# Kernel optimization log

Hardware: AMD Instinct MI355X
Metric: run time of the kernel (lower is better)

The kernel has to match this reference:

```python
import jax, jax.numpy as jnp
import numpy as np

L, D, H, HK, DH, F, V, T, B = 8, 1024, 16, 4, 64, 2816, 32000, 1024, 2
G = H // HK
THETA = 10000.0
EPS = 1e-6
SCALE = DH ** -0.5


def _rope_tables(t, dh, theta):
    inv = 1.0 / theta ** (jnp.arange(0, dh, 2, dtype=jnp.float32) / dh)  # [dh/2]
    ang = jnp.arange(t, dtype=jnp.float32)[:, None] * inv[None, :]       # [T, dh/2]
    return jnp.cos(ang), jnp.sin(ang)


def _apply_rope(x, cos, sin):
    # x: [B, T, h, DH] -> rotate pairs (even, odd)
    xr = x.reshape(*x.shape[:-1], DH // 2, 2)
    x0, x1 = xr[..., 0], xr[..., 1]
    c = cos[None, :, None, :]
    s = sin[None, :, None, :]
    out = jnp.stack([x0 * c - x1 * s, x0 * s + x1 * c], axis=-1)
    return out.reshape(*x.shape)


def _rmsnorm(x, w):
    var = jnp.mean(x * x, axis=-1, keepdims=True)
    return x * jax.lax.rsqrt(var + EPS) * w


def setup_inputs() -> dict:
    key = jax.random.key(0)
    ks = jax.random.split(key, 10)
    s = 0.02
    return {
        "ids": jax.random.randint(ks[0], (B, T), 0, V),
        "emb": jax.random.normal(ks[1], (V, D), jnp.float32) * s,
        "qw": jax.random.normal(ks[2], (L, H * DH, D), jnp.float32) * s,
        "kw": jax.random.normal(ks[3], (L, HK * DH, D), jnp.float32) * s,
        "vw": jax.random.normal(ks[4], (L, HK * DH, D), jnp.float32) * s,
        "ow": jax.random.normal(ks[5], (L, D, D), jnp.float32) * s,
        "w1": jax.random.normal(ks[6], (L, F, D), jnp.float32) * s,
        "w2": jax.random.normal(ks[7], (L, D, F), jnp.float32) * s,
        "w3": jax.random.normal(ks[8], (L, F, D), jnp.float32) * s,
        "n1": jnp.ones((L, D), jnp.float32),
        "n2": jnp.ones((L, D), jnp.float32),
        "nf": jnp.ones((D,), jnp.float32),
    }


def _forward(ids, emb, qw, kw, vw, ow, w1, w2, w3, n1, n2, nf):
    cos, sin = _rope_tables(T, DH, THETA)
    causal = jnp.tril(jnp.ones((T, T), dtype=bool))  # [T, T]
    x = emb[ids]  # [B, T, D]
    for l in range(L):
        xn = _rmsnorm(x, n1[l])
        q = jnp.einsum("btd,ed->bte", xn, qw[l]).reshape(B, T, H, DH)
        k = jnp.einsum("btd,ed->bte", xn, kw[l]).reshape(B, T, HK, DH)
        v = jnp.einsum("btd,ed->bte", xn, vw[l]).reshape(B, T, HK, DH)
        q = _apply_rope(q, cos, sin)
        k = _apply_rope(k, cos, sin)
        # GQA: group query heads over shared kv heads
        qg = q.transpose(0, 2, 1, 3).reshape(B, HK, G, T, DH)
        kh = k.transpose(0, 2, 1, 3)  # [B, HK, T, DH]
        vh = v.transpose(0, 2, 1, 3)
        scores = jnp.einsum("bkgtd,bksd->bkgts", qg, kh) * SCALE
        scores = jnp.where(causal, scores, -jnp.inf)
        p = jax.nn.softmax(scores, axis=-1)
        out = jnp.einsum("bkgts,bksd->bkgtd", p, vh)
        out = out.reshape(B, H, T, DH).transpose(0, 2, 1, 3).reshape(B, T, D)
        x = x + jnp.einsum("btd,ed->bte", out, ow[l])
        xn2 = _rmsnorm(x, n2[l])
        h1 = jnp.einsum("btd,fd->btf", xn2, w1[l])
        h3 = jnp.einsum("btd,fd->btf", xn2, w3[l])
        x = x + jnp.einsum("btf,df->btd", jax.nn.silu(h1) * h3, w2[l])
    x = _rmsnorm(x, nf)
    logits = jnp.einsum("btd,vd->btv", x, emb)  # tied lm_head
    return logits


def reference(ids, emb, qw, kw, vw, ow, w1, w2, w3, n1, n2, nf):
    return _forward(ids, emb, qw, kw, vw, ow, w1, w2, w3, n1, n2, nf)
```

## Files before the change

kernel.cpp:

```cpp
#include <hip/hip_runtime.h>
#include <math.h>

#define L_ 8
#define D_ 1024
#define H_ 16
#define HK_ 4
#define DH_ 64
#define F_ 2816
#define V_ 32000
#define T_ 1024
#define B_ 2
#define M_ (B_*T_)
#define SCALE_ 0.125f

typedef unsigned short u16;
typedef unsigned int   u32;
typedef __attribute__((ext_vector_type(4))) float  f32x4;
typedef __attribute__((ext_vector_type(8))) short  bf16x8;
typedef __attribute__((ext_vector_type(4))) unsigned short u16x4;
typedef __attribute__((ext_vector_type(4))) unsigned int   u32x4;

__device__ __forceinline__ float bf2f(u16 h) {
    union { u32 u; float f; } v; v.u = ((u32)h) << 16; return v.f;
}
__device__ __forceinline__ u16 f2bf(float f) {
    union { float f; u32 u; } v; v.f = f;
    u32 r = v.u + 0x7fffu + ((v.u >> 16) & 1u);
    return (u16)(r >> 16);
}

__device__ __forceinline__ void gl_lds16(const void* g, void* l) {
    __builtin_amdgcn_global_load_lds(
        (const __attribute__((address_space(1))) unsigned int*)g,
        (__attribute__((address_space(3))) unsigned int*)l,
        16, 0, 0);
}

template<int N> __device__ __forceinline__ void vm_wait() {
    if constexpr (N == 0) asm volatile("s_waitcnt vmcnt(0)" ::: "memory");
    else if constexpr (N == 3) asm volatile("s_waitcnt vmcnt(3)" ::: "memory");
    else if constexpr (N == 4) asm volatile("s_waitcnt vmcnt(4)" ::: "memory");
    else if constexpr (N == 6) asm volatile("s_waitcnt vmcnt(6)" ::: "memory");
    else if constexpr (N == 8) asm volatile("s_waitcnt vmcnt(8)" ::: "memory");
}

template<int BM, int EPI>
__global__ __launch_bounds__(256)
void gemm3_k(const u16* __restrict__ A, int K,
             const u16* __restrict__ W, int N,
             float* __restrict__ Of, u16* __restrict__ Ob,
             const float* __restrict__ tc, const float* __restrict__ ts)
{
    constexpr int FM = BM / 32;
    constexpr int FN = 4;
    constexpr int GM = M_ / BM;
    constexpr int IPA = BM / 64;
    constexpr int LPT = IPA + 2;
    __shared__ u16 sA[3 * BM * 32];
    __shared__ u16 sB[3 * 128 * 32];

    const int tid  = threadIdx.x;
    const int lane = tid & 63, wv = tid >> 6;
    const int wm = wv >> 1, wn = wv & 1;
    const int l15 = lane & 15, lhi = lane >> 4;
    const int m0 = wm * (BM / 2), n0 = wn * 64;

    const int nwg = gridDim.x;
    const int q8 = nwg >> 3, r8 = nwg & 7;
    const int xcd = blockIdx.x & 7, off8 = blockIdx.x >> 3;
    const int wgid = (xcd < r8 ? xcd * (q8 + 1) : r8 * (q8 + 1) + (xcd - r8) * q8) + off8;
    const int tM = wgid % GM, tN = wgid / GM;

    const int srow = lane >> 2;
    const int scol = (lane & 3) * 8;

    const u16* Abase = A + (size_t)(tM * BM) * K;
    const u16* Wbase = W + (size_t)(tN * 128) * K;

    f32x4 acc[FM][FN];
#pragma unroll
    for (int i = 0; i < FM; ++i)
#pragma unroll
        for (int j = 0; j < FN; ++j) acc[i][j] = f32x4{0.f, 0.f, 0.f, 0.f};

    auto stage = [&](int t, int buf) {
        const int kt = t << 5;
        u16* sa = sA + buf * (BM * 32);
        u16* sb = sB + buf * (128 * 32);
#pragma unroll
        for (int i = 0; i < IPA; ++i) {
            int c = wv * IPA + i;
            gl_lds16(Abase + (size_t)(c * 16 + srow) * K + kt + scol, sa + c * 512);
        }
#pragma unroll
        for (int i = 0; i < 2; ++i) {
            int c = wv * 2 + i;
            gl_lds16(Wbase + (size_t)(c * 16 + srow) * K + kt + scol, sb + c * 512);
        }
    };

    const int nt = K >> 5;
    stage(0, 0);
    stage(1, 1);

    for (int t = 0; t < nt; ++t) {
        if (t + 2 < nt) { stage(t + 2, (t + 2) % 3); vm_wait<2 * LPT>(); }
        else if (t + 1 < nt) vm_wait<LPT>();
        else vm_wait<0>();
        __builtin_amdgcn_s_barrier();

        const u16* sa = sA + (t % 3) * (BM * 32);
        const u16* sb = sB + (t % 3) * (128 * 32);
        bf16x8 av[FM], bv[FN];
#pragma unroll
        for (int i = 0; i < FM; ++i)
            av[i] = *(const bf16x8*)&sa[(m0 + i * 16 + l15) * 32 + lhi * 8];
#pragma unroll
        for (int j = 0; j < FN; ++j)
            bv[j] = *(const bf16x8*)&sb[(n0 + j * 16 + l15) * 32 + lhi * 8];
#pragma unroll
        for (int i = 0; i < FM; ++i)
#pragma unroll
            for (int j = 0; j < FN; ++j)
                acc[i][j] = __builtin_amdgcn_mfma_f32_16x16x32_bf16(
                    av[i], bv[j], acc[i][j], 0, 0, 0);

        if (t + 1 < nt) {
            asm volatile("s_waitcnt lgkmcnt(0)" ::: "memory");
            __builtin_amdgcn_s_barrier();
        }
    }

#pragma unroll
    for (int i = 0; i < FM; ++i)
#pragma unroll
        for (int j = 0; j < FN; ++j) {
            size_t gm = (size_t)tM * BM + m0 + i * 16 + lhi * 4;
            size_t gn = (size_t)tN * 128 + n0 + j * 16 + l15;
#pragma unroll
            for (int r = 0; r < 4; ++r) {
                float v = acc[i][j][r];
                size_t idx = (gm + r) * (size_t)N + gn;
                if (EPI == 0) {
                    Ob[idx] = f2bf(v);
                } else if (EPI == 1) {
                    Of[idx] = v;
                } else if (EPI == 2) {
                    Of[idx] += v;
                } else if (EPI == 3) {
                    float b = __shfl_xor(v, 1);
                    if ((lane & 1) == 0) {
                        float s = v / (1.0f + expf(-v));
                        Ob[(gm + r) * (size_t)F_ + (gn >> 1)] = f2bf(s * b);
                    }
                } else {
                    float b = __shfl_xor(v, 1);
                    if ((int)gn < 1280) {
                        int dd = (int)gn & 63;
                        int jj = dd >> 1;
                        int tt = (int)(gm + r) & (T_ - 1);
                        float c = tc[tt * 32 + jj], s = ts[tt * 32 + jj];
                        float ro = ((dd & 1) == 0) ? (v * c - b * s) : (b * s + v * c);
                        Ob[idx] = f2bf(ro);
                    } else {
                        Ob[idx] = f2bf(v);
                    }
                }
            }
        }
}

__global__ __launch_bounds__(256)
void cvt_k(const float* __restrict__ src, u16* __restrict__ dst,
           unsigned long long sStride, unsigned long long dStride)
{
    int l = blockIdx.y;
    size_t i = ((size_t)blockIdx.x * 256 + threadIdx.x) * 4;
    f32x4 v = *(const f32x4*)(src + l * sStride + i);
    u16x4 o;
    o.x = f2bf(v.x); o.y = f2bf(v.y); o.z = f2bf(v.z); o.w = f2bf(v.w);
    *(u16x4*)(dst + l * dStride + i) = o;
}

__global__ __launch_bounds__(256)
void cvt_il_k(const float* __restrict__ src, u16* __restrict__ dst,
              unsigned long long sStride, unsigned long long dStride, int off)
{
    int f = blockIdx.x, l = blockIdx.y;
    int i = threadIdx.x * 4;
    f32x4 v = *(const f32x4*)(src + l * sStride + (size_t)f * D_ + i);
    u16x4 o;
    o.x = f2bf(v.x); o.y = f2bf(v.y); o.z = f2bf(v.z); o.w = f2bf(v.w);
    *(u16x4*)(dst + l * dStride + (size_t)(2 * f + off) * D_ + i) = o;
}

template<int BM, int BN, int EPI, int NW>
__global__ __launch_bounds__(256)
void gemm_k(const u16* __restrict__ A, int K,
            const float* __restrict__ W0, const float* __restrict__ W1p,
            const float* __restrict__ W2p, int N0, int N1, int N,
            float* __restrict__ Of, u16* __restrict__ Ob)
{
    constexpr int FM = BM / 32;
    constexpr int FN = BN / 32;
    constexpr int LS = 40;
    __shared__ u16 sA[BM * LS];
    __shared__ u16 sB[BN * LS];

    const int tid  = threadIdx.x;
    const int lane = tid & 63, wv = tid >> 6;
    const int wm = wv >> 1, wn = wv & 1;
    const int l15 = lane & 15, lhi = lane >> 4;
    const int m0 = wm * (BM / 2), n0 = wn * (BN / 2);
    const int tM = blockIdx.y, tN = blockIdx.x;

    f32x4 acc[FM][FN];
#pragma unroll
    for (int i = 0; i < FM; ++i)
#pragma unroll
        for (int j = 0; j < FN; ++j) acc[i][j] = f32x4{0.f, 0.f, 0.f, 0.f};

    for (int kt = 0; kt < K; kt += 32) {
#pragma unroll
        for (int i = 0; i < BM / 64; ++i) {
            int cid = tid + i * 256;
            int row = cid >> 2, kc = cid & 3;
            const u16* src = A + (size_t)(tM * BM + row) * K + kt + kc * 8;
            *(u32x4*)&sA[row * LS + kc * 8] = *(const u32x4*)src;
        }
#pragma unroll
        for (int i = 0; i < BN / 32; ++i) {
            int cid = tid + i * 256;
            int row = cid >> 3, kc = cid & 7;
            int n = tN * BN + row;
            const float* wr;
            if (NW == 1)      wr = W0 + (size_t)n * K;
            else if (NW == 2) wr = (n < N0) ? (W0 + (size_t)n * K)
                                            : (W1p + (size_t)(n - N0) * K);
            else              wr = (n < N0) ? (W0 + (size_t)n * K)
                               : (n < N0 + N1) ? (W1p + (size_t)(n - N0) * K)
                                               : (W2p + (size_t)(n - N0 - N1) * K);
            f32x4 v = *(const f32x4*)(wr + kt + kc * 4);
            u16x4 o;
            o.x = f2bf(v.x); o.y = f2bf(v.y); o.z = f2bf(v.z); o.w = f2bf(v.w);
            *(u16x4*)&sB[row * LS + kc * 4] = o;
        }
        __syncthreads();

        bf16x8 av[FM], bv[FN];
#pragma unroll
        for (int i = 0; i < FM; ++i)
            av[i] = *(const bf16x8*)&sA[(m0 + i * 16 + l15) * LS + lhi * 8];
#pragma unroll
        for (int j = 0; j < FN; ++j)
            bv[j] = *(const bf16x8*)&sB[(n0 + j * 16 + l15) * LS + lhi * 8];
#pragma unroll
        for (int i = 0; i < FM; ++i)
#pragma unroll
            for (int j = 0; j < FN; ++j)
                acc[i][j] = __builtin_amdgcn_mfma_f32_16x16x32_bf16(
                    av[i], bv[j], acc[i][j], 0, 0, 0);
        __syncthreads();
    }

#pragma unroll
    for (int i = 0; i < FM; ++i)
#pragma unroll
        for (int j = 0; j < FN; ++j) {
            size_t gm = (size_t)tM * BM + m0 + i * 16 + lhi * 4;
            size_t gn = (size_t)tN * BN + n0 + j * 16 + l15;
#pragma unroll
            for (int r = 0; r < 4; ++r) {
                float v = acc[i][j][r];
                size_t idx = (gm + r) * (size_t)N + gn;
                if (EPI == 0)      Ob[idx] = f2bf(v);
                else if (EPI == 1) Of[idx] = v;
                else               Of[idx] += v;
            }
        }
}

__global__ __launch_bounds__(256)
void vtrans_k(const u16* __restrict__ qkv, u16* __restrict__ vt)
{
    int rr = blockIdx.x;
    int d = rr & 63, hk = (rr >> 6) & 3, b = rr >> 8;
    int t = threadIdx.x * 4;
    const u16* base = qkv + (size_t)(b * T_ + t) * 1536 + 1280 + hk * 64 + d;
    u16 a0 = base[0];
    u16 a1 = base[1536];
    u16 a2 = base[3072];
    u16 a3 = base[4608];
    u16x4 o; o.x = a0; o.y = a1; o.z = a2; o.w = a3;
    *(u16x4*)(vt + (size_t)rr * T_ + t) = o;
}

__global__ __launch_bounds__(256)
void attn2_k(const u16* __restrict__ qkv, const u16* __restrict__ vt,
             u16* __restrict__ attn)
{
    const int qt = blockIdx.x, h = blockIdx.y, b = blockIdx.z;
    const int hk = h >> 2;
    const int tid = threadIdx.x;
    const int lane = tid & 63, w = tid >> 6;
    const int l15 = lane & 15, lhi = lane >> 4;

    __shared__ u16 sK[128 * 64];
    __shared__ u16 sVT[64 * 128];
    __shared__ u16 sP[4][16 * 136];

    const int q0 = qt * 64;
    const u16* qptr = qkv + (size_t)(b * T_ + q0 + w * 16 + l15) * 1536 + h * 64 + lhi * 8;
    bf16x8 aq0 = *(const bf16x8*)qptr;
    bf16x8 aq1 = *(const bf16x8*)(qptr + 32);

    f32x4 accO[4];
#pragma unroll
    for (int d = 0; d < 4; ++d) accO[d] = f32x4{0.f, 0.f, 0.f, 0.f};
    float m_r[4] = {-1e30f, -1e30f, -1e30f, -1e30f};
    float l_r[4] = {0.f, 0.f, 0.f, 0.f};
    const int myq = q0 + w * 16 + lhi * 4;
    const int qmaxw = q0 + w * 16 + 15;
    u16* sPw = sP[w];

    const int ntiles = (qt + 2) >> 1;
    const u16* vtb = vt + (size_t)((b * HK_ + hk) * DH_) * T_;
    const int L = lane;

    for (int kt = 0; kt < ntiles; ++kt) {
        const int t0 = kt * 128;
#pragma unroll
        for (int i = 0; i < 4; ++i) {
            int c = w * 4 + i;
            int row = c * 8 + (L >> 3);
            int p = L & 7;
            const u16* src = qkv + (size_t)(b * T_ + t0 + row) * 1536 + 1024 + hk * 64
                             + ((p ^ (row & 7)) * 8);
            gl_lds16(src, sK + c * 512);
        }
#pragma unroll
        for (int i = 0; i < 4; ++i) {
            int c = w * 4 + i;
            int row = c * 4 + (L >> 4);
            int p = L & 15;
            const u16* src = vtb + (size_t)row * T_ + t0 + ((p ^ (row & 15)) * 8);
            gl_lds16(src, sVT + c * 512);
        }
        asm volatile("s_waitcnt vmcnt(0)" ::: "memory");
        __syncthreads();

        const bool lastt = (kt == ntiles - 1);

        f32x4 accS[8];
#pragma unroll
        for (int nf = 0; nf < 8; ++nf)
            accS[nf] = f32x4{-1e30f, -1e30f, -1e30f, -1e30f};
#pragma unroll
        for (int pk = 0; pk < 4; ++pk) {
            if (t0 + pk * 32 > qmaxw) continue;
            f32x4 s0 = f32x4{0.f, 0.f, 0.f, 0.f};
            f32x4 s1 = f32x4{0.f, 0.f, 0.f, 0.f};
#pragma unroll
            for (int kk = 0; kk < 2; ++kk) {
                bf16x8 aqs = kk ? aq1 : aq0;
                int r0 = (pk * 2) * 16 + l15;
                int r1 = (pk * 2 + 1) * 16 + l15;
                int ls = kk * 4 + lhi;
                bf16x8 b0 = *(const bf16x8*)&sK[r0 * 64 + ((ls ^ (r0 & 7)) * 8)];
                bf16x8 b1 = *(const bf16x8*)&sK[r1 * 64 + ((ls ^ (r1 & 7)) * 8)];
                s0 = __builtin_amdgcn_mfma_f32_16x16x32_bf16(aqs, b0, s0, 0, 0, 0);
                s1 = __builtin_amdgcn_mfma_f32_16x16x32_bf16(aqs, b1, s1, 0, 0, 0);
            }
#pragma unroll
            for (int r = 0; r < 4; ++r) {
                float v0 = s0[r] * SCALE_;
                float v1 = s1[r] * SCALE_;
                if (lastt) {
                    int kp0 = t0 + (pk * 2) * 16 + l15;
                    int kp1 = kp0 + 16;
                    if (kp0 > myq + r) v0 = -1e30f;
                    if (kp1 > myq + r) v1 = -1e30f;
                }
                accS[pk * 2][r] = v0;
                accS[pk * 2 + 1][r] = v1;
            }
        }

        float sc[4];
#pragma unroll
        for (int r = 0; r < 4; ++r) {
            float mx = accS[0][r];
#pragma unroll
            for (int nf = 1; nf < 8; ++nf) mx = fmaxf(mx, accS[nf][r]);
#pragma unroll
            for (int off = 1; off < 16; off <<= 1) mx = fmaxf(mx, __shfl_xor(mx, off));
            float mn = fmaxf(m_r[r], mx);
            sc[r] = expf(m_r[r] - mn);
            m_r[r] = mn;
        }
        float rs[4] = {0.f, 0.f, 0.f, 0.f};
#pragma unroll
        for (int pk = 0; pk < 4; ++pk) {
            if (t0 + pk * 32 > qmaxw) continue;
#pragma unroll
            for (int g = 0; g < 2; ++g) {
                int nf = pk * 2 + g;
#pragma unroll
                for (int r = 0; r < 4; ++r) {
                    float p = expf(accS[nf][r] - m_r[r]);
                    accS[nf][r] = p;
                    rs[r] += p;
                }
            }
        }
#pragma unroll
        for (int r = 0; r < 4; ++r) {
#pragma unroll
            for (int off = 1; off < 16; off <<= 1) rs[r] += __shfl_xor(rs[r], off);
            l_r[r] = l_r[r] * sc[r] + rs[r];
        }
#pragma unroll
        for (int d = 0; d < 4; ++d)
#pragma unroll
            for (int r = 0; r < 4; ++r) accO[d][r] *= sc[r];

#pragma unroll
        for (int pk = 0; pk < 4; ++pk) {
            if (t0 + pk * 32 > qmaxw) continue;
#pragma unroll
            for (int g = 0; g < 2; ++g) {
                int nf = pk * 2 + g;
#pragma unroll
                for (int r = 0; r < 4; ++r)
                    sPw[(lhi * 4 + r) * 136 + nf * 16 + l15] = f2bf(accS[nf][r]);
            }
        }

#pragma unroll
        for (int kk = 0; kk < 4; ++kk) {
            if (t0 + kk * 32 > qmaxw) continue;
            bf16x8 pas = *(const bf16x8*)&sPw[l15 * 136 + kk * 32 + lhi * 8];
#pragma unroll
            for (int nf = 0; nf < 4; ++nf) {
                int row = nf * 16 + l15;
                int ls = kk * 4 + lhi;
                bf16x8 bvv = *(const bf16x8*)&sVT[row * 128 + ((ls ^ (row & 15)) * 8)];
                accO[nf] = __builtin_amdgcn_mfma_f32_16x16x32_bf16(pas, bvv, accO[nf], 0, 0, 0);
            }
        }
        __syncthreads();
    }

#pragma unroll
    for (int d = 0; d < 4; ++d)
#pragma unroll
        for (int r = 0; r < 4; ++r) {
            int row = q0 + w * 16 + lhi * 4 + r;
            float o = accO[d][r] / l_r[r];
            attn[(size_t)(b * T_ + row) * 1024 + h * 64 + d * 16 + l15] = f2bf(o);
        }
}

__global__ __launch_bounds__(256)
void attn_k(const u16* __restrict__ qkv, u16* __restrict__ attn)
{
    const int qt = blockIdx.x, h = blockIdx.y, b = blockIdx.z;
    const int hk = h >> 2;
    const int tid = threadIdx.x;
    const int lane = tid & 63, w = tid >> 6;
    const int l15 = lane & 15, lhi = lane >> 4;
    __shared__ u16 sK[64 * 72];
    __shared__ u16 sVT[64 * 74];
    __shared__ u16 sP[4 * 16 * 72];

    const int q0 = qt * 64;
    const u16* qptr = qkv + (size_t)(b * T_ + q0 + w * 16 + l15) * 1536 + h * 64 + lhi * 8;
    bf16x8 aq0 = *(const bf16x8*)qptr;
    bf16x8 aq1 = *(const bf16x8*)(qptr + 32);

    f32x4 accO[4];
#pragma unroll
    for (int d = 0; d < 4; ++d) accO[d] = f32x4{0.f, 0.f, 0.f, 0.f};
    float m_r[4] = {-1e30f, -1e30f, -1e30f, -1e30f};
    float l_r[4] = {0.f, 0.f, 0.f, 0.f};
    const int myq = q0 + w * 16 + lhi * 4;
    u16* sPw = sP + w * 16 * 72;

    for (int kt = 0; kt <= qt; ++kt) {
#pragma unroll
        for (int i = 0; i < 2; ++i) {
            int cid = tid + i * 256;
            int r = cid >> 3, kc = cid & 7;
            const u16* src = qkv + (size_t)(b * T_ + kt * 64 + r) * 1536 + 1024 + hk * 64 + kc * 8;
            *(u32x4*)&sK[r * 72 + kc * 8] = *(const u32x4*)src;
        }
#pragma unroll
        for (int i = 0; i < 2; ++i) {
            int cid = tid + i * 256;
            int tt = cid >> 3, dc = cid & 7;
            const u16* src = qkv + (size_t)(b * T_ + kt * 64 + tt) * 1536 + 1280 + hk * 64 + dc * 8;
            bf16x8 vv = *(const bf16x8*)src;
#pragma unroll
            for (int j = 0; j < 8; ++j) sVT[(dc * 8 + j) * 74 + tt] = (u16)vv[j];
        }
        __syncthreads();

        f32x4 accS[4];
#pragma unroll
        for (int nf = 0; nf < 4; ++nf) accS[nf] = f32x4{0.f, 0.f, 0.f, 0.f};
#pragma unroll
        for (int s = 0; s < 2; ++s) {
            bf16x8 aqs = s ? aq1 : aq0;
#pragma unroll
            for (int nf = 0; nf < 4; ++nf) {
                bf16x8 bk = *(const bf16x8*)&sK[(nf * 16 + l15) * 72 + s * 32 + lhi * 8];
                accS[nf] = __builtin_amdgcn_mfma_f32_16x16x32_bf16(aqs, bk, accS[nf], 0, 0, 0);
            }
        }
#pragma unroll
        for (int nf = 0; nf < 4; ++nf)
#pragma unroll
            for (int r = 0; r < 4; ++r) {
                float v = accS[nf][r] * SCALE_;
                if (kt == qt) {
                    int kp = kt * 64 + nf * 16 + l15;
                    if (kp > myq + r) v = -1e30f;
                }
                accS[nf][r] = v;
            }
        float sc[4];
#pragma unroll
        for (int r = 0; r < 4; ++r) {
            float mx = fmaxf(fmaxf(accS[0][r], accS[1][r]), fmaxf(accS[2][r], accS[3][r]));
#pragma unroll
            for (int off = 1; off < 16; off <<= 1) mx = fmaxf(mx, __shfl_xor(mx, off));
            float mn = fmaxf(m_r[r], mx);
            sc[r] = expf(m_r[r] - mn);
            m_r[r] = mn;
        }
        float rs[4] = {0.f, 0.f, 0.f, 0.f};
#pragma unroll
        for (int nf = 0; nf < 4; ++nf)
#pragma unroll
            for (int r = 0; r < 4; ++r) {
                float p = expf(accS[nf][r] - m_r[r]);
                accS[nf][r] = p;
                rs[r] += p;
            }
#pragma unroll
        for (int r = 0; r < 4; ++r) {
#pragma unroll
            for (int off = 1; off < 16; off <<= 1) rs[r] += __shfl_xor(rs[r], off);
            l_r[r] = l_r[r] * sc[r] + rs[r];
        }
#pragma unroll
        for (int d = 0; d < 4; ++d)
#pragma unroll
            for (int r = 0; r < 4; ++r) accO[d][r] *= sc[r];

#pragma unroll
        for (int nf = 0; nf < 4; ++nf)
#pragma unroll
            for (int r = 0; r < 4; ++r)
                sPw[(lhi * 4 + r) * 72 + nf * 16 + l15] = f2bf(accS[nf][r]);
        bf16x8 pa0 = *(const bf16x8*)&sPw[l15 * 72 + lhi * 8];
        bf16x8 pa1 = *(const bf16x8*)&sPw[l15 * 72 + 32 + lhi * 8];
#pragma unroll
        for (int s = 0; s < 2; ++s) {
            bf16x8 pas = s ? pa1 : pa0;
#pragma unroll
            for (int d = 0; d < 4; ++d) {
                bf16x8 bvv = *(const bf16x8*)&sVT[(d * 16 + l15) * 74 + s * 32 + lhi * 8];
                accO[d] = __builtin_amdgcn_mfma_f32_16x16x32_bf16(pas, bvv, accO[d], 0, 0, 0);
            }
        }
        __syncthreads();
    }

#pragma unroll
    for (int d = 0; d < 4; ++d)
#pragma unroll
        for (int r = 0; r < 4; ++r) {
            int row = q0 + w * 16 + lhi * 4 + r;
            float o = accO[d][r] / l_r[r];
            attn[(size_t)(b * T_ + row) * 1024 + h * 64 + d * 16 + l15] = f2bf(o);
        }
}

__global__ __launch_bounds__(256)
void gather_k(const int* __restrict__ ids, const float* __restrict__ emb,
              float* __restrict__ x)
{
    int m = blockIdx.x, tid = threadIdx.x;
    int id = ids[m];
    *(f32x4*)(x + (size_t)m * D_ + tid * 4) =
        *(const f32x4*)(emb + (size_t)id * D_ + tid * 4);
}

__global__ __launch_bounds__(256)
void rmsnorm_k(const float* __restrict__ x, const float* __restrict__ g,
               u16* __restrict__ out)
{
    const int row = blockIdx.x, tid = threadIdx.x;
    const float* xr = x + (size_t)row * D_;
    f32x4 v = *(const f32x4*)(xr + tid * 4);
    float ss = v.x * v.x + v.y * v.y + v.z * v.z + v.w * v.w;
#pragma unroll
    for (int off = 32; off >= 1; off >>= 1) ss += __shfl_xor(ss, off);
    __shared__ float red[4];
    if ((tid & 63) == 0) red[tid >> 6] = ss;
    __syncthreads();
    float tot = red[0] + red[1] + red[2] + red[3];
    float rr = rsqrtf(tot * (1.0f / D_) + 1e-6f);
    f32x4 wv = *(const f32x4*)(g + tid * 4);
    u16x4 o;
    o.x = f2bf(v.x * rr * wv.x); o.y = f2bf(v.y * rr * wv.y);
    o.z = f2bf(v.z * rr * wv.z); o.w = f2bf(v.w * rr * wv.w);
    *(u16x4*)(out + (size_t)row * D_ + tid * 4) = o;
}

__global__ __launch_bounds__(256)
void rope_tab_k(float* __restrict__ tc, float* __restrict__ ts)
{
    int idx = blockIdx.x * 256 + threadIdx.x;
    int t = idx >> 5, j = idx & 31;
    float inv = powf(10000.0f, -(float)j * (1.0f / 32.0f));
    float ang = (float)t * inv;
    tc[idx] = cosf(ang);
    ts[idx] = sinf(ang);
}

__global__ __launch_bounds__(256)
void silu_f32_k(const float* __restrict__ h13, u16* __restrict__ hh)
{
    int m = blockIdx.y;
    int f = blockIdx.x * 256 + threadIdx.x;
    float a = h13[(size_t)m * (2 * F_) + f];
    float c = h13[(size_t)m * (2 * F_) + F_ + f];
    float s = a / (1.0f + expf(-a));
    hh[(size_t)m * F_ + f] = f2bf(s * c);
}

__global__ __launch_bounds__(640)
void rope_slow_k(u16* __restrict__ qkv)
{
    int m = blockIdx.x;
    int c2 = threadIdx.x;
    int col = (c2 < 512) ? (c2 * 2) : (1024 + (c2 - 512) * 2);
    int d = col & 63;
    int t = m & (T_ - 1);
    float ang = (float)t * powf(10000.0f, -(float)d / 64.0f);
    float cs = cosf(ang), sn = sinf(ang);
    u16* p = qkv + (size_t)m * 1536 + col;
    float x0 = bf2f(p[0]), x1 = bf2f(p[1]);
    p[0] = f2bf(x0 * cs - x1 * sn);
    p[1] = f2bf(x0 * sn + x1 * cs);
}

extern "C" void kernel_launch(void* const* d_in, const int* in_sizes, int n_in,
                              void* d_out, int out_size, void* d_ws, size_t ws_size,
                              hipStream_t stream)
{
    const int*   ids = (const int*)d_in[0];
    const float* emb = (const float*)d_in[1];
    const float* qw  = (const float*)d_in[2];
    const float* kw  = (const float*)d_in[3];
    const float* vw  = (const float*)d_in[4];
    const float* ow  = (const float*)d_in[5];
    const float* w1  = (const float*)d_in[6];
    const float* w2  = (const float*)d_in[7];
    const float* w3  = (const float*)d_in[8];
    const float* n1  = (const float*)d_in[9];
    const float* n2  = (const float*)d_in[10];
    const float* nfw = (const float*)d_in[11];
    float* out = (float*)d_out;
    char*  ws  = (char*)d_ws;

    float* x    = (float*)(ws);
    u16*   xn   = (u16*)(ws + 8388608ULL);
    u16*   qkvb = (u16*)(ws + 12582912ULL);
    u16*   attnb= (u16*)(ws + 18874368ULL);
    u16*   hh   = (u16*)(ws + 46137344ULL);
    float* ropec= (float*)(ws + 57671680ULL);
    float* ropes= (float*)(ws + 57802752ULL);
    u16*   embb = (u16*)(ws + 57933824ULL);
    u16*   wqkv = (u16*)(ws + 123469824ULL);
    u16*   wob  = (u16*)(ws + 148635648ULL);
    u16*   w13b = (u16*)(ws + 165412864ULL);
    u16*   w2b  = (u16*)(ws + 257687552ULL);
    u16*   vtb  = (u16*)(ws + 303824896ULL);
    const unsigned long long NEED = 304873472ULL;

    if (ws_size >= NEED) {
        cvt_k<<<dim3(32000, 1), 256, 0, stream>>>(emb, embb, 0, 0);
        cvt_k<<<dim3(1024, L_), 256, 0, stream>>>(qw, wqkv,            1048576ULL, 1572864ULL);
        cvt_k<<<dim3(256,  L_), 256, 0, stream>>>(kw, wqkv + 1048576,  262144ULL,  1572864ULL);
        cvt_k<<<dim3(256,  L_), 256, 0, stream>>>(vw, wqkv + 1310720,  262144ULL,  1572864ULL);
        cvt_k<<<dim3(1024, L_), 256, 0, stream>>>(ow, wob,             1048576ULL, 1048576ULL);
        cvt_il_k<<<dim3(2816, L_), 256, 0, stream>>>(w1, w13b, 2883584ULL, 5767168ULL, 0);
        cvt_il_k<<<dim3(2816, L_), 256, 0, stream>>>(w3, w13b, 2883584ULL, 5767168ULL, 1);
        cvt_k<<<dim3(2816, L_), 256, 0, stream>>>(w2, w2b,             2883584ULL, 2883584ULL);
        rope_tab_k<<<T_ * 32 / 256, 256, 0, stream>>>(ropec, ropes);

        gather_k<<<M_, 256, 0, stream>>>(ids, emb, x);

        for (int l = 0; l < L_; ++l) {
            rmsnorm_k<<<M_, 256, 0, stream>>>(x, n1 + l * D_, xn);
            gemm3_k<64, 4><<<32 * 12, 256, 0, stream>>>(
                xn, D_, wqkv + (size_t)l * 1572864, 1536, nullptr, qkvb, ropec, ropes);
            vtrans_k<<<B_ * HK_ * DH_, 256, 0, stream>>>(qkvb, vtb);
            attn2_k<<<dim3(T_ / 64, H_, B_), 256, 0, stream>>>(qkvb, vtb, attnb);
            gemm3_k<64, 2><<<32 * 8, 256, 0, stream>>>(
                attnb, D_, wob + (size_t)l * 1048576, 1024, x, nullptr, nullptr, nullptr);
            rmsnorm_k<<<M_, 256, 0, stream>>>(x, n2 + l * D_, xn);
            gemm3_k<128, 3><<<16 * 44, 256, 0, stream>>>(
                xn, D_, w13b + (size_t)l * 5767168, 5632, nullptr, hh, nullptr, nullptr);
            gemm3_k<64, 2><<<32 * 8, 256, 0, stream>>>(
                hh, F_, w2b + (size_t)l * 2883584, 1024, x, nullptr, nullptr, nullptr);
        }

        rmsnorm_k<<<M_, 256, 0, stream>>>(x, nfw, xn);
        gemm3_k<128, 1><<<16 * 250, 256, 0, stream>>>(
            xn, D_, embb, V_, out, nullptr, nullptr, nullptr);
        return;
    }

    float* h13f = (float*)(ws + 23068672ULL);
    u16*   hhf  = (u16*)(ws + 69206016ULL);
    gather_k<<<M_, 256, 0, stream>>>(ids, emb, x);

    for (int l = 0; l < L_; ++l) {
        rmsnorm_k<<<M_, 256, 0, stream>>>(x, n1 + l * D_, xn);
        gemm_k<128, 64, 0, 3><<<dim3(24, 16), 256, 0, stream>>>(
            xn, D_,
            qw + (size_t)l * H_ * DH_ * D_,
            kw + (size_t)l * HK_ * DH_ * D_,
            vw + (size_t)l * HK_ * DH_ * D_,
            1024, 256, 1536, nullptr, qkvb);
        rope_slow_k<<<M_, 640, 0, stream>>>(qkvb);
        attn_k<<<dim3(T_ / 64, H_, B_), 256, 0, stream>>>(qkvb, attnb);
        gemm_k<128, 64, 2, 1><<<dim3(16, 16), 256, 0, stream>>>(
            attnb, D_, ow + (size_t)l * D_ * D_, nullptr, nullptr,
            0, 0, D_, x, nullptr);
        rmsnorm_k<<<M_, 256, 0, stream>>>(x, n2 + l * D_, xn);
        gemm_k<128, 128, 1, 2><<<dim3(44, 16), 256, 0, stream>>>(
            xn, D_, w1 + (size_t)l * F_ * D_, w3 + (size_t)l * F_ * D_, nullptr,
            F_, 0, 2 * F_, h13f, nullptr);
        silu_f32_k<<<dim3(11, M_), 256, 0, stream>>>(h13f, hhf);
        gemm_k<128, 64, 2, 1><<<dim3(16, 16), 256, 0, stream>>>(
            hhf, F_, w2 + (size_t)l * D_ * F_, nullptr, nullptr,
            0, 0, D_, x, nullptr);
    }

    rmsnorm_k<<<M_, 256, 0, stream>>>(x, nfw, xn);
    gemm_k<128, 128, 1, 1><<<dim3(250, 16), 256, 0, stream>>>(
        xn, D_, emb, nullptr, nullptr, 0, 0, V_, out, nullptr);
}
```

Measured before the change: 2.025 ms.

## Switch GEMMs to double-buffered BN-templated kernel, fuse V transpose into QKV epilogue

The triple-buffered GEMM is replaced by a double-buffered version that takes a configurable N tile. The QKV, O-projection and W2 GEMMs now use 64x64 tiles, which doubles their grid size. The QKV epilogue writes V already transposed into the vt buffer, so the separate vtrans kernel launch is gone. Attention blocks are now launched in reverse query-tile order so the longer causal tiles start first. The shallower pipeline waits on vmcnt(0) every iteration, which may expose more memory latency.

```diff
diff --git a/kernel.cpp b/kernel.cpp
--- a/kernel.cpp
+++ b/kernel.cpp
@@ -36,34 +36,26 @@
         16, 0, 0);
 }
 
-template<int N> __device__ __forceinline__ void vm_wait() {
-    if constexpr (N == 0) asm volatile("s_waitcnt vmcnt(0)" ::: "memory");
-    else if constexpr (N == 3) asm volatile("s_waitcnt vmcnt(3)" ::: "memory");
-    else if constexpr (N == 4) asm volatile("s_waitcnt vmcnt(4)" ::: "memory");
-    else if constexpr (N == 6) asm volatile("s_waitcnt vmcnt(6)" ::: "memory");
-    else if constexpr (N == 8) asm volatile("s_waitcnt vmcnt(8)" ::: "memory");
-}
-
-template<int BM, int EPI>
-__global__ __launch_bounds__(256)
-void gemm3_k(const u16* __restrict__ A, int K,
+template<int BM, int BN, int EPI>
+__global__ __launch_bounds__(256)
+void gemm2_k(const u16* __restrict__ A, int K,
              const u16* __restrict__ W, int N,
              float* __restrict__ Of, u16* __restrict__ Ob,
              const float* __restrict__ tc, const float* __restrict__ ts)
 {
     constexpr int FM = BM / 32;
-    constexpr int FN = 4;
+    constexpr int FN = BN / 32;
     constexpr int GM = M_ / BM;
     constexpr int IPA = BM / 64;
-    constexpr int LPT = IPA + 2;
-    __shared__ u16 sA[3 * BM * 32];
-    __shared__ u16 sB[3 * 128 * 32];
+    constexpr int IPB = BN / 64;
+    __shared__ u16 sA[2 * BM * 32];
+    __shared__ u16 sB[2 * BN * 32];
 
     const int tid  = threadIdx.x;
     const int lane = tid & 63, wv = tid >> 6;
     const int wm = wv >> 1, wn = wv & 1;
     const int l15 = lane & 15, lhi = lane >> 4;
-    const int m0 = wm * (BM / 2), n0 = wn * 64;
+    const int m0 = wm * (BM / 2), n0 = wn * (BN / 2);
 
     const int nwg = gridDim.x;
     const int q8 = nwg >> 3, r8 = nwg & 7;
@@ -75,7 +67,7 @@
     const int scol = (lane & 3) * 8;
 
     const u16* Abase = A + (size_t)(tM * BM) * K;
-    const u16* Wbase = W + (size_t)(tN * 128) * K;
+    const u16* Wbase = W + (size_t)(tN * BN) * K;
 
     f32x4 acc[FM][FN];
 #pragma unroll
@@ -83,34 +75,32 @@
 #pragma unroll
         for (int j = 0; j < FN; ++j) acc[i][j] = f32x4{0.f, 0.f, 0.f, 0.f};
 
-    auto stage = [&](int t, int buf) {
-        const int kt = t << 5;
+    auto stage = [&](int kt, int buf) {
         u16* sa = sA + buf * (BM * 32);
-        u16* sb = sB + buf * (128 * 32);
+        u16* sb = sB + buf * (BN * 32);
 #pragma unroll
         for (int i = 0; i < IPA; ++i) {
             int c = wv * IPA + i;
             gl_lds16(Abase + (size_t)(c * 16 + srow) * K + kt + scol, sa + c * 512);
         }
 #pragma unroll
-        for (int i = 0; i < 2; ++i) {
-            int c = wv * 2 + i;
+        for (int i = 0; i < IPB; ++i) {
+            int c = wv * IPB + i;
             gl_lds16(Wbase + (size_t)(c * 16 + srow) * K + kt + scol, sb + c * 512);
         }
     };
 
     const int nt = K >> 5;
     stage(0, 0);
-    stage(1, 1);
-
+    asm volatile("s_waitcnt vmcnt(0)" ::: "memory");
+    __syncthreads();
+
+    int cur = 0;
     for (int t = 0; t < nt; ++t) {
-        if (t + 2 < nt) { stage(t + 2, (t + 2) % 3); vm_wait<2 * LPT>(); }
-        else if (t + 1 < nt) vm_wait<LPT>();
-        else vm_wait<0>();
-        __builtin_amdgcn_s_barrier();
-
-        const u16* sa = sA + (t % 3) * (BM * 32);
-        const u16* sb = sB + (t % 3) * (128 * 32);
+        if (t + 1 < nt) stage((t + 1) << 5, cur ^ 1);
+
+        const u16* sa = sA + cur * (BM * 32);
+        const u16* sb = sB + cur * (BN * 32);
         bf16x8 av[FM], bv[FN];
 #pragma unroll
         for (int i = 0; i < FM; ++i)
@@ -126,8 +116,9 @@
                     av[i], bv[j], acc[i][j], 0, 0, 0);
 
         if (t + 1 < nt) {
-            asm volatile("s_waitcnt lgkmcnt(0)" ::: "memory");
-            __builtin_amdgcn_s_barrier();
+            asm volatile("s_waitcnt vmcnt(0)" ::: "memory");
+            __syncthreads();
+            cur ^= 1;
         }
     }
 
@@ -136,7 +127,7 @@
 #pragma unroll
         for (int j = 0; j < FN; ++j) {
             size_t gm = (size_t)tM * BM + m0 + i * 16 + lhi * 4;
-            size_t gn = (size_t)tN * 128 + n0 + j * 16 + l15;
+            size_t gn = (size_t)tN * BN + n0 + j * 16 + l15;
 #pragma unroll
             for (int r = 0; r < 4; ++r) {
                 float v = acc[i][j][r];
@@ -155,15 +146,20 @@
                     }
                 } else {
                     float b = __shfl_xor(v, 1);
-                    if ((int)gn < 1280) {
-                        int dd = (int)gn & 63;
+                    int gni = (int)gn;
+                    int gmr = (int)(gm + r);
+                    if (gni < 1280) {
+                        int dd = gni & 63;
                         int jj = dd >> 1;
-                        int tt = (int)(gm + r) & (T_ - 1);
+                        int tt = gmr & (T_ - 1);
                         float c = tc[tt * 32 + jj], s = ts[tt * 32 + jj];
                         float ro = ((dd & 1) == 0) ? (v * c - b * s) : (b * s + v * c);
                         Ob[idx] = f2bf(ro);
                     } else {
-                        Ob[idx] = f2bf(v);
+                        int vc = gni - 1280;
+                        int hk = vc >> 6, dd = vc & 63;
+                        int bb = gmr >> 10, tt = gmr & (T_ - 1);
+                        ((u16*)Of)[((size_t)((bb * HK_ + hk) * DH_ + dd)) * T_ + tt] = f2bf(v);
                     }
                 }
             }
@@ -281,25 +277,11 @@
 }
 
 __global__ __launch_bounds__(256)
-void vtrans_k(const u16* __restrict__ qkv, u16* __restrict__ vt)
-{
-    int rr = blockIdx.x;
-    int d = rr & 63, hk = (rr >> 6) & 3, b = rr >> 8;
-    int t = threadIdx.x * 4;
-    const u16* base = qkv + (size_t)(b * T_ + t) * 1536 + 1280 + hk * 64 + d;
-    u16 a0 = base[0];
-    u16 a1 = base[1536];
-    u16 a2 = base[3072];
-    u16 a3 = base[4608];
-    u16x4 o; o.x = a0; o.y = a1; o.z = a2; o.w = a3;
-    *(u16x4*)(vt + (size_t)rr * T_ + t) = o;
-}
-
-__global__ __launch_bounds__(256)
 void attn2_k(const u16* __restrict__ qkv, const u16* __restrict__ vt,
              u16* __restrict__ attn)
 {
-    const int qt = blockIdx.x, h = blockIdx.y, b = blockIdx.z;
+    const int qt = gridDim.x - 1 - blockIdx.x;
+    const int h = blockIdx.y, b = blockIdx.z;
     const int hk = h >> 2;
     const int tid = threadIdx.x;
     const int lane = tid & 63, w = tid >> 6;
@@ -706,21 +688,20 @@
 
         for (int l = 0; l < L_; ++l) {
             rmsnorm_k<<<M_, 256, 0, stream>>>(x, n1 + l * D_, xn);
-            gemm3_k<64, 4><<<32 * 12, 256, 0, stream>>>(
-                xn, D_, wqkv + (size_t)l * 1572864, 1536, nullptr, qkvb, ropec, ropes);
-            vtrans_k<<<B_ * HK_ * DH_, 256, 0, stream>>>(qkvb, vtb);
+            gemm2_k<64, 64, 4><<<32 * 24, 256, 0, stream>>>(
+                xn, D_, wqkv + (size_t)l * 1572864, 1536, (float*)vtb, qkvb, ropec, ropes);
             attn2_k<<<dim3(T_ / 64, H_, B_), 256, 0, stream>>>(qkvb, vtb, attnb);
-            gemm3_k<64, 2><<<32 * 8, 256, 0, stream>>>(
+            gemm2_k<64, 64, 2><<<32 * 16, 256, 0, stream>>>(
                 attnb, D_, wob + (size_t)l * 1048576, 1024, x, nullptr, nullptr, nullptr);
             rmsnorm_k<<<M_, 256, 0, stream>>>(x, n2 + l * D_, xn);
-            gemm3_k<128, 3><<<16 * 44, 256, 0, stream>>>(
+            gemm2_k<128, 128, 3><<<16 * 44, 256, 0, stream>>>(
                 xn, D_, w13b + (size_t)l * 5767168, 5632, nullptr, hh, nullptr, nullptr);
-            gemm3_k<64, 2><<<32 * 8, 256, 0, stream>>>(
+            gemm2_k<64, 64, 2><<<32 * 16, 256, 0, stream>>>(
                 hh, F_, w2b + (size_t)l * 2883584, 1024, x, nullptr, nullptr, nullptr);
         }
 
         rmsnorm_k<<<M_, 256, 0, stream>>>(x, nfw, xn);
-        gemm3_k<128, 1><<<16 * 250, 256, 0, stream>>>(
+        gemm2_k<128, 128, 1><<<16 * 250, 256, 0, stream>>>(
             xn, D_, embb, V_, out, nullptr, nullptr, nullptr);
         return;
     }
```

New measurement: 1.825 ms. 9.9% less time.
